# Performance work log

Measured on AMD Instinct MI355X. Metric: run time of the kernel, lower is better.

## Reference

```python
import jax, jax.numpy as jnp
import numpy as np

N_NODES = 50000
N_EDGES = 1_600_000
IN_DIM = 128
HID = 64


def gcn_conv(x, src, dst, w, W, b, n):
    # PyG GCNConv(normalize=True, add_self_loops=True):
    # add self loops with weight 1, sym-normalize, x@W (no bias in lin), scatter-add, +bias
    loop = jnp.arange(n)
    s = jnp.concatenate([src, loop])
    d = jnp.concatenate([dst, loop])
    ww = jnp.concatenate([w, jnp.ones((n,), w.dtype)])
    deg = jax.ops.segment_sum(ww, d, num_segments=n)                 # [n]
    dis = jnp.where(deg > 0, jax.lax.rsqrt(deg), 0.0)                # deg^{-1/2}, inf->0
    norm = dis[s] * ww * dis[d]                                      # [E+n]
    h = x @ W                                                        # [n, out]
    msg = h[s] * norm[:, None]                                       # gather + scale
    out = jax.ops.segment_sum(msg, d, num_segments=n)                # scatter-add at dst
    return out + b


def setup_inputs() -> dict:
    key = jax.random.key(0)
    ks = jax.random.split(key, 9)
    X = jax.random.normal(ks[0], (N_NODES, IN_DIM), dtype=jnp.float32)
    edge_index = jax.random.randint(ks[1], (2, N_EDGES), 0, N_NODES, dtype=jnp.int64)
    edge_weight = jax.random.uniform(ks[2], (N_EDGES,), dtype=jnp.float32)
    s1 = 1.0 / np.sqrt(IN_DIM)
    s2 = 1.0 / np.sqrt(HID)
    W1 = jax.random.uniform(ks[3], (IN_DIM, HID), jnp.float32, -s1, s1)
    b1 = jax.random.uniform(ks[4], (HID,), jnp.float32, -s1, s1)
    W2 = jax.random.uniform(ks[5], (HID, HID), jnp.float32, -s2, s2)
    b2 = jax.random.uniform(ks[6], (HID,), jnp.float32, -s2, s2)
    Wl = jax.random.uniform(ks[7], (HID, 1), jnp.float32, -s2, s2)
    bl = jax.random.uniform(ks[8], (1,), jnp.float32, -s2, s2)
    return {"X": X, "edge_index": edge_index, "edge_weight": edge_weight,
            "W1": W1, "b1": b1, "W2": W2, "b2": b2, "Wl": Wl, "bl": bl}


def reference(X, edge_index, edge_weight, W1, b1, W2, b2, Wl, bl):
    n = X.shape[0]
    src, dst = edge_index[0], edge_index[1]
    h = jax.nn.relu(gcn_conv(X, src, dst, edge_weight, W1, b1, n))
    # F.dropout(p=0.2) is identity in eval mode
    h = jax.nn.relu(gcn_conv(h, src, dst, edge_weight, W2, b2, n))
    return jax.nn.sigmoid(h @ Wl + bl).squeeze(1)   # [n]
```

## Files before the change

kernel.cpp:

```cpp
#include <hip/hip_runtime.h>

typedef float f32x2 __attribute__((ext_vector_type(2)));

#define A2B 1024
#define A2T 512
#define STG 3200

__device__ __forceinline__ long ld_idx(const void* idx, long pos, int is64) {
  return is64 ? (long)((const long long*)idx)[pos]
              : (long)((const int*)idx)[pos];
}

__device__ __forceinline__ int detect_is64(const void* idx) {
  const unsigned long long* p = (const unsigned long long*)idx;
  unsigned long long v = p[threadIdx.x & 63];
  return (__ballot((v >> 32) != 0ull) == 0ull) ? 1 : 0;
}

__device__ __forceinline__ int swz_group(int bid, int GP) {
  int r = bid & 7, q = bid >> 3;
  int j = q / GP;
  int i = q - j * GP;
  return (r + 8 * j) * GP + i;
}

__device__ __forceinline__ void scan256(unsigned* sh, unsigned* wsums, int t) {
  unsigned v = 0;
  if (t < 256) {
    v = sh[t];
#pragma unroll
    for (int off = 1; off < 64; off <<= 1) {
      unsigned u = __shfl_up(v, off, 64);
      if ((t & 63) >= off) v += u;
    }
    if ((t & 63) == 63) wsums[t >> 6] = v;
  }
  __syncthreads();
  if (t < 256) {
    unsigned add = 0;
    int wid = t >> 6;
#pragma unroll
    for (int i = 0; i < 3; ++i) if (i < wid) add += wsums[i];
    sh[t] = v + add;
  }
  __syncthreads();
}

__device__ __forceinline__ uint4 pack16_fp8(const float* acc) {
  uint4 o;
  unsigned v;
  v = 0;
  v = __builtin_amdgcn_cvt_pk_fp8_f32(acc[0],  acc[1],  v, false);
  v = __builtin_amdgcn_cvt_pk_fp8_f32(acc[2],  acc[3],  v, true);
  o.x = v; v = 0;
  v = __builtin_amdgcn_cvt_pk_fp8_f32(acc[4],  acc[5],  v, false);
  v = __builtin_amdgcn_cvt_pk_fp8_f32(acc[6],  acc[7],  v, true);
  o.y = v; v = 0;
  v = __builtin_amdgcn_cvt_pk_fp8_f32(acc[8],  acc[9],  v, false);
  v = __builtin_amdgcn_cvt_pk_fp8_f32(acc[10], acc[11], v, true);
  o.z = v; v = 0;
  v = __builtin_amdgcn_cvt_pk_fp8_f32(acc[12], acc[13], v, false);
  v = __builtin_amdgcn_cvt_pk_fp8_f32(acc[14], acc[15], v, true);
  o.w = v;
  return o;
}

__global__ __launch_bounds__(256) void k_front(const void* __restrict__ idx,
                                               unsigned* __restrict__ histT,
                                               long E, int chunk, unsigned M) {
  __shared__ unsigned cnt[256];
  const int t = threadIdx.x;
  const int b = blockIdx.x;
  const int is64 = detect_is64(idx);
  cnt[t] = 0;
  __syncthreads();
  const long e0 = (long)b * chunk;
  long e1 = e0 + chunk; if (e1 > E) e1 = E;
  for (long e = e0 + t; e < e1; e += 256) {
    unsigned d = (unsigned)ld_idx(idx, E + e, is64);
    atomicAdd(&cnt[__umulhi(d, M)], 1u);
  }
  __syncthreads();
  histT[(size_t)t * A2B + b] = cnt[t];
}

__global__ __launch_bounds__(256) void k_colscan(const unsigned* __restrict__ histT,
                                                 unsigned* __restrict__ baseT,
                                                 unsigned* __restrict__ colsum) {
  __shared__ unsigned sh[256], wsums[4];
  const int k = blockIdx.x, t = threadIdx.x;
  const uint4 v = ((const uint4*)(histT + (size_t)k * A2B))[t];
  unsigned s = v.x + v.y + v.z + v.w;
  sh[t] = s;
  __syncthreads();
  scan256(sh, wsums, t);
  unsigned excl = sh[t] - s;
  uint4 o;
  o.x = excl;
  o.y = excl + v.x;
  o.z = o.y + v.y;
  o.w = o.z + v.z;
  ((uint4*)(baseT + (size_t)k * A2B))[t] = o;
  if (t == 255) colsum[k] = sh[255];
}

__global__ __launch_bounds__(A2T) void k_bucket(const void* __restrict__ idx,
                                                const float* __restrict__ w,
                                                const unsigned* __restrict__ baseT,
                                                const unsigned* __restrict__ colsum,
                                                uint2* __restrict__ recs,
                                                long E, int chunk, unsigned M,
                                                const float* __restrict__ X,
                                                const float* __restrict__ W1,
                                                unsigned char* __restrict__ h, int n) {
  __shared__ uint2 stage[4096];
  __shared__ unsigned cnt[256], lofs[256], lbase[256], bcol[256], scanb[256], wsums[4];
  const int t = threadIdx.x;
  if (blockIdx.x >= A2B) {
    float* Ws = (float*)stage;
    for (int i = t; i < 2048; i += A2T)
      ((float4*)Ws)[i] = ((const float4*)W1)[i];
    __syncthreads();
    int gid = (blockIdx.x - A2B) * A2T + t;
    int node = gid >> 2;
    int fg = (gid & 3) * 16;
    if (node >= n) return;
    const float4* xr4 = (const float4*)(X + (size_t)node * 128);
    float acc[16];
#pragma unroll
    for (int f = 0; f < 16; ++f) acc[f] = 0.0f;
    for (int k4 = 0; k4 < 32; ++k4) {
      float4 x = xr4[k4];
#pragma unroll
      for (int kk = 0; kk < 4; ++kk) {
        float xv = (kk == 0) ? x.x : (kk == 1) ? x.y : (kk == 2) ? x.z : x.w;
        const float4* wrow = (const float4*)(Ws + (k4 * 4 + kk) * 64 + fg);
#pragma unroll
        for (int f4 = 0; f4 < 4; ++f4) {
          float4 wv = wrow[f4];
          acc[f4 * 4 + 0] = fmaf(xv, wv.x, acc[f4 * 4 + 0]);
          acc[f4 * 4 + 1] = fmaf(xv, wv.y, acc[f4 * 4 + 1]);
          acc[f4 * 4 + 2] = fmaf(xv, wv.z, acc[f4 * 4 + 2]);
          acc[f4 * 4 + 3] = fmaf(xv, wv.w, acc[f4 * 4 + 3]);
        }
      }
    }
    *(uint4*)(h + (size_t)node * 64 + fg) = pack16_fp8(acc);
    return;
  }
  const int b = blockIdx.x;
  const long e0 = (long)b * chunk;
  long e1 = e0 + chunk; if (e1 > E) e1 = E;
  const int m = (int)(e1 - e0);
  const int is64 = detect_is64(idx);
  if (t < 256) scanb[t] = colsum[t];
  __syncthreads();
  scan256(scanb, wsums, t);
  if (t < 256) {
    bcol[t] = (scanb[t] - colsum[t]) + baseT[(size_t)t * A2B + b];
    cnt[t] = 0;
  }
  __syncthreads();
  unsigned short dc[4]; unsigned char kc[4];
  int nk = 0;
  for (long e = e0 + t; e < e1; e += A2T, ++nk) {
    unsigned d = (unsigned)ld_idx(idx, E + e, is64);
    unsigned kb = __umulhi(d, M);
    dc[nk] = (unsigned short)d; kc[nk] = (unsigned char)kb;
    atomicAdd(&cnt[kb], 1u);
  }
  __syncthreads();
  if (t < 256) scanb[t] = cnt[t];
  __syncthreads();
  scan256(scanb, wsums, t);
  if (t < 256) { unsigned ex = scanb[t] - cnt[t]; lbase[t] = ex; lofs[t] = ex; }
  __syncthreads();
  nk = 0;
  for (long e = e0 + t; e < e1; e += A2T, ++nk) {
    unsigned s = (unsigned)ld_idx(idx, e, is64);
    float wv = w[e];
    unsigned kb = kc[nk];
    unsigned pos = atomicAdd(&lofs[kb], 1u);
    stage[pos] = make_uint2(s | ((unsigned)dc[nk] << 16), __float_as_uint(wv));
  }
  __syncthreads();
  for (int i = t; i < m; i += A2T) {
    uint2 r = stage[i];
    unsigned kb = __umulhi(r.x >> 16, M);
    recs[bcol[kb] + (unsigned)i - lbase[kb]] = r;
  }
}

__global__ __launch_bounds__(1024) void k_bp(const uint2* __restrict__ recs,
                                             const unsigned* __restrict__ colsum,
                                             int* __restrict__ rowptr,
                                             float* __restrict__ dis,
                                             float2* __restrict__ edges,
                                             int n, int dwidth, long E) {
  __shared__ float wsum[256];
  __shared__ unsigned cnt[256], lofs[256], scanb[256], wsums[4];
  const int k = blockIdx.x, t = threadIdx.x;
  const int d0 = k * dwidth;
  if (t < 256) scanb[t] = colsum[t];
  __syncthreads();
  scan256(scanb, wsums, t);
  const int r1 = (int)scanb[k];
  const int r0 = r1 - (int)colsum[k];
  if (t < 256) { wsum[t] = 0.0f; cnt[t] = 0; }
  __syncthreads();
  const int m = r1 - r0;
  for (int i = t; i < m; i += 1024) {
    uint2 r = recs[r0 + i];
    int dl = (int)(r.x >> 16) - d0;
    atomicAdd(&cnt[dl], 1u);
    atomicAdd(&wsum[dl], __uint_as_float(r.y));
  }
  __syncthreads();
  if (t < 256) scanb[t] = cnt[t];
  __syncthreads();
  scan256(scanb, wsums, t);
  if (t < 256) {
    unsigned ex = scanb[t] - cnt[t];
    lofs[t] = (unsigned)r0 + ex;
    int d = d0 + t;
    if (t < dwidth && d < n) {
      rowptr[d] = r0 + (int)ex;
      dis[d] = rsqrtf(1.0f + wsum[t]);
    }
  }
  if (k == gridDim.x - 1 && t == 0) rowptr[n] = (int)E;
  __syncthreads();
  for (int i = t; i < m; i += 1024) {
    uint2 r = recs[r0 + i];
    unsigned pos = atomicAdd(&lofs[(int)(r.x >> 16) - d0], 1u);
    edges[pos] = make_float2(__uint_as_float(r.x & 0xffffu), __uint_as_float(r.y));
  }
}

__device__ __forceinline__ void gather_acc(const unsigned char* __restrict__ h,
                                           const float* __restrict__ dis,
                                           const float2* __restrict__ edges,
                                           int beg, int end, int eg, int fl,
                                           float* acc) {
  f32x2 a0 = {0.0f, 0.0f}, a1 = {0.0f, 0.0f}, a2 = {0.0f, 0.0f}, a3 = {0.0f, 0.0f};
  const unsigned char* hf = h + fl * 8;
  for (int base = beg; base < end; base += 48) {
    float2 rv[12];
#pragma unroll
    for (int s = 0; s < 12; ++s) {
      int idx = base + s * 4 + eg;
      rv[s] = edges[min(idx, end - 1)];
    }
    int sj[12];
    float nj[12];
#pragma unroll
    for (int s = 0; s < 12; ++s) {
      sj[s] = __float_as_int(rv[s].x);
      nj[s] = rv[s].y * dis[sj[s]];
    }
    uint2 hv[12];
#pragma unroll
    for (int s = 0; s < 12; ++s)
      hv[s] = *(const uint2*)(hf + (size_t)sj[s] * 64);
#pragma unroll
    for (int s = 0; s < 12; ++s) {
      float w = (base + s * 4 + eg < end) ? nj[s] : 0.0f;
      f32x2 nj2 = {w, w};
      a0 += __builtin_amdgcn_cvt_pk_f32_fp8(hv[s].x, false) * nj2;
      a1 += __builtin_amdgcn_cvt_pk_f32_fp8(hv[s].x, true)  * nj2;
      a2 += __builtin_amdgcn_cvt_pk_f32_fp8(hv[s].y, false) * nj2;
      a3 += __builtin_amdgcn_cvt_pk_f32_fp8(hv[s].y, true)  * nj2;
    }
  }
  acc[0] = a0[0]; acc[1] = a0[1]; acc[2] = a1[0]; acc[3] = a1[1];
  acc[4] = a2[0]; acc[5] = a2[1]; acc[6] = a3[0]; acc[7] = a3[1];
#pragma unroll
  for (int off = 8; off < 32; off <<= 1)
#pragma unroll
    for (int i = 0; i < 8; ++i) acc[i] += __shfl_xor(acc[i], off);
}

__device__ __forceinline__ void add_bias_self(const unsigned char* __restrict__ h,
                                              const float* __restrict__ b,
                                              int node, int fl, float s0, float* acc) {
  uint2 hv = *(const uint2*)(h + (size_t)node * 64 + fl * 8);
  f32x2 q0 = __builtin_amdgcn_cvt_pk_f32_fp8(hv.x, false);
  f32x2 q1 = __builtin_amdgcn_cvt_pk_f32_fp8(hv.x, true);
  f32x2 q2 = __builtin_amdgcn_cvt_pk_f32_fp8(hv.y, false);
  f32x2 q3 = __builtin_amdgcn_cvt_pk_f32_fp8(hv.y, true);
  float hs[8] = {q0[0], q0[1], q1[0], q1[1], q2[0], q2[1], q3[0], q3[1]};
  float4 bv0 = *(const float4*)(b + fl * 8);
  float4 bv1 = *(const float4*)(b + fl * 8 + 4);
  float bb[8] = {bv0.x, bv0.y, bv0.z, bv0.w, bv1.x, bv1.y, bv1.z, bv1.w};
  float s2 = s0 * s0;
#pragma unroll
  for (int i = 0; i < 8; ++i) acc[i] += bb[i] + hs[i] * s2;
}

__global__ __launch_bounds__(256) void k_gather_mid(const unsigned char* __restrict__ h,
                                                    const float* __restrict__ dis,
                                                    const float2* __restrict__ edges,
                                                    const int* __restrict__ rowptr,
                                                    const float* __restrict__ b1,
                                                    const float* __restrict__ W2,
                                                    unsigned char* __restrict__ h2,
                                                    int n, int GP) {
  __shared__ float W2s[64 * 64];
  __shared__ float xs[8 * 64];
  const int t = threadIdx.x;
  for (int i = t; i < 1024; i += 256)
    ((float4*)W2s)[i] = ((const float4*)W2)[i];
  int lane = t & 63;
  int l32 = lane & 31;
  int fl = lane & 7;
  int eg = (lane >> 3) & 3;
  int nl = t >> 5;
  const int g = swz_group(blockIdx.x, GP);
  int node = g * 8 + nl;
  int beg = 0, end = 0; float s0 = 0.0f;
  if (node < n) { beg = rowptr[node]; end = rowptr[node + 1]; s0 = dis[node]; }
  float acc[8];
  gather_acc(h, dis, edges, beg, end, eg, fl, acc);
  if (node < n) {
#pragma unroll
    for (int i = 0; i < 8; ++i) acc[i] *= s0;
    add_bias_self(h, b1, node, fl, s0, acc);
    if (eg == 0) {
#pragma unroll
      for (int i = 0; i < 8; ++i) xs[nl * 64 + fl * 8 + i] = fmaxf(acc[i], 0.0f);
    }
  }
  __syncthreads();
  int tl = l32;
  int node2 = g * 8 + (t >> 5);
  if (node2 >= n) return;
  const float* xrow = xs + (t >> 5) * 64;
  int f = tl * 2;
  float a0 = 0.0f, a1 = 0.0f;
#pragma unroll 8
  for (int k = 0; k < 64; ++k) {
    float xk = xrow[k];
    f32x2 wv = *(const f32x2*)(W2s + k * 64 + f);
    a0 = fmaf(xk, wv[0], a0);
    a1 = fmaf(xk, wv[1], a1);
  }
  unsigned v = __builtin_amdgcn_cvt_pk_fp8_f32(a0, a1, 0u, false);
  *(unsigned short*)(h2 + (size_t)node2 * 64 + f) = (unsigned short)v;
}

__global__ __launch_bounds__(256) void k_gather_fin(const unsigned char* __restrict__ h,
                                                    const float* __restrict__ dis,
                                                    const float2* __restrict__ edges,
                                                    const int* __restrict__ rowptr,
                                                    const float* __restrict__ b2,
                                                    const float* __restrict__ Wl,
                                                    const float* __restrict__ bl,
                                                    float* __restrict__ out,
                                                    int n, int GP) {
  int lane = threadIdx.x & 63;
  int l32 = lane & 31;
  int fl = lane & 7;
  int eg = (lane >> 3) & 3;
  const int g = swz_group(blockIdx.x, GP);
  int node = g * 8 + (int)(threadIdx.x >> 5);
  if (node >= n) return;
  int beg = rowptr[node], end = rowptr[node + 1];
  float s0 = dis[node];
  float acc[8];
  gather_acc(h, dis, edges, beg, end, eg, fl, acc);
#pragma unroll
  for (int i = 0; i < 8; ++i) acc[i] *= s0;
  add_bias_self(h, b2, node, fl, s0, acc);
  float4 wl0 = *(const float4*)(Wl + fl * 8);
  float4 wl1 = *(const float4*)(Wl + fl * 8 + 4);
  float wl[8] = {wl0.x, wl0.y, wl0.z, wl0.w, wl1.x, wl1.y, wl1.z, wl1.w};
  float v = 0.0f;
#pragma unroll
  for (int i = 0; i < 8; ++i) v += fmaxf(acc[i], 0.0f) * wl[i];
#pragma unroll
  for (int off = 1; off < 8; off <<= 1) v += __shfl_xor(v, off);
  if (l32 == 0) out[node] = 1.0f / (1.0f + expf(-(v + bl[0])));
}

extern "C" void kernel_launch(void* const* d_in, const int* in_sizes, int n_in,
                              void* d_out, int out_size, void* d_ws, size_t ws_size,
                              hipStream_t stream) {
  const float* X  = (const float*)d_in[0];
  const void*  EI = d_in[1];
  const float* EW = (const float*)d_in[2];
  const float* W1 = (const float*)d_in[3];
  const float* b1 = (const float*)d_in[4];
  const float* W2 = (const float*)d_in[5];
  const float* b2 = (const float*)d_in[6];
  const float* Wl = (const float*)d_in[7];
  const float* bl = (const float*)d_in[8];
  float* out = (float*)d_out;

  const int  n = in_sizes[0] / 128;
  const long E = (long)in_sizes[1] / 2;

  const int chunk  = (int)((E + A2B - 1) / A2B);
  const int dwidth = (((n + 255) / 256) + 7) & ~7;
  const int GP     = dwidth >> 3;
  const unsigned M = (unsigned)((0x100000000ULL + (unsigned)dwidth - 1) / (unsigned)dwidth);

  auto align = [](size_t x) { return (x + 255) & ~(size_t)255; };
  char* ws = (char*)d_ws;
  size_t off = 0;
  float*         dis    = (float*)(ws + off);         off += align((size_t)n * 4);
  int*           rowptr = (int*)(ws + off);           off += align((size_t)(n + 1) * 4);
  unsigned*      colsum = (unsigned*)(ws + off);      off += align(256 * 4);
  unsigned*      histT  = (unsigned*)(ws + off);      off += align((size_t)A2B * 256 * 4);
  unsigned*      baseT  = (unsigned*)(ws + off);      off += align((size_t)A2B * 256 * 4);
  uint2*         recs   = (uint2*)(ws + off);         off += align((size_t)E * 8);
  float2*        edges  = (float2*)(ws + off);        off += align((size_t)E * 8);
  unsigned char* A      = (unsigned char*)(ws + off); off += align((size_t)n * 64);
  unsigned char* A2     = (unsigned char*)(ws + off); off += align((size_t)n * 64);

  const int nbW  = 32 * dwidth;
  const int nbG  = (n * 4 + A2T - 1) / A2T;

  k_front<<<A2B, dim3(256), 0, stream>>>(EI, histT, E, chunk, M);
  k_colscan<<<256, 256, 0, stream>>>(histT, baseT, colsum);
  k_bucket<<<A2B + nbG, dim3(A2T), 0, stream>>>(EI, EW, baseT, colsum, recs, E, chunk, M,
                                                X, W1, A, n);
  k_bp<<<256, dim3(1024), 0, stream>>>(recs, colsum, rowptr, dis, edges, n, dwidth, E);

  k_gather_mid<<<nbW, dim3(256), 0, stream>>>(A, dis, edges, rowptr, b1, W2, A2, n, GP);
  k_gather_fin<<<nbW, dim3(256), 0, stream>>>(A2, dis, edges, rowptr, b2, Wl, bl, out, n, GP);
}
```

Baseline: 214.8 us.

## Fuse graph preprocessing kernels into one cooperative kernel with grid syncs

Merges the histogram, column scan, bucket scatter and per-bucket CSR build kernels into a single cooperative launch, separated by grid.sync() barriers. The X@W1 projection is folded into the first phase of the first blocks. The edge chunking drops from 1024 to 512 blocks of 512 threads, so each block handles about twice as many edges. The aim is to remove kernel launch gaps and inter-kernel drain, at the cost of grid-wide barrier overhead, lower block-level parallelism, and the matmul now sitting in front of the first barrier.

```diff
diff --git a/kernel.cpp b/kernel.cpp
--- a/kernel.cpp
+++ b/kernel.cpp
@@ -1,9 +1,12 @@
 #include <hip/hip_runtime.h>
+#include <hip/hip_cooperative_groups.h>
+
+namespace cg = cooperative_groups;
 
 typedef float f32x2 __attribute__((ext_vector_type(2)));
 
-#define A2B 1024
-#define A2T 512
+#define A2B 512
+#define CPT 512
 #define STG 3200
 
 __device__ __forceinline__ long ld_idx(const void* idx, long pos, int is64) {
@@ -65,94 +68,93 @@
   return o;
 }
 
-__global__ __launch_bounds__(256) void k_front(const void* __restrict__ idx,
-                                               unsigned* __restrict__ histT,
-                                               long E, int chunk, unsigned M) {
-  __shared__ unsigned cnt[256];
+__global__ __launch_bounds__(CPT, 4) void k_prep(const void* __restrict__ idx,
+                                                 const float* __restrict__ w,
+                                                 unsigned* __restrict__ histT,
+                                                 unsigned* __restrict__ baseT,
+                                                 unsigned* __restrict__ colsum,
+                                                 uint2* __restrict__ recs,
+                                                 int* __restrict__ rowptr,
+                                                 float* __restrict__ dis,
+                                                 float2* __restrict__ edges,
+                                                 const float* __restrict__ X,
+                                                 const float* __restrict__ W1,
+                                                 unsigned char* __restrict__ h,
+                                                 long E, int chunk, unsigned M,
+                                                 int n, int dwidth, int nbG1) {
+  __shared__ uint2 stage[4096];
+  __shared__ unsigned cnt[256], lofs[256], lbase[256], bcol[256], scanb[256], wsums[8];
+  __shared__ float wsum[256];
+  cg::grid_group grid = cg::this_grid();
   const int t = threadIdx.x;
   const int b = blockIdx.x;
   const int is64 = detect_is64(idx);
-  cnt[t] = 0;
-  __syncthreads();
-  const long e0 = (long)b * chunk;
-  long e1 = e0 + chunk; if (e1 > E) e1 = E;
-  for (long e = e0 + t; e < e1; e += 256) {
-    unsigned d = (unsigned)ld_idx(idx, E + e, is64);
-    atomicAdd(&cnt[__umulhi(d, M)], 1u);
-  }
-  __syncthreads();
-  histT[(size_t)t * A2B + b] = cnt[t];
-}
-
-__global__ __launch_bounds__(256) void k_colscan(const unsigned* __restrict__ histT,
-                                                 unsigned* __restrict__ baseT,
-                                                 unsigned* __restrict__ colsum) {
-  __shared__ unsigned sh[256], wsums[4];
-  const int k = blockIdx.x, t = threadIdx.x;
-  const uint4 v = ((const uint4*)(histT + (size_t)k * A2B))[t];
-  unsigned s = v.x + v.y + v.z + v.w;
-  sh[t] = s;
-  __syncthreads();
-  scan256(sh, wsums, t);
-  unsigned excl = sh[t] - s;
-  uint4 o;
-  o.x = excl;
-  o.y = excl + v.x;
-  o.z = o.y + v.y;
-  o.w = o.z + v.z;
-  ((uint4*)(baseT + (size_t)k * A2B))[t] = o;
-  if (t == 255) colsum[k] = sh[255];
-}
-
-__global__ __launch_bounds__(A2T) void k_bucket(const void* __restrict__ idx,
-                                                const float* __restrict__ w,
-                                                const unsigned* __restrict__ baseT,
-                                                const unsigned* __restrict__ colsum,
-                                                uint2* __restrict__ recs,
-                                                long E, int chunk, unsigned M,
-                                                const float* __restrict__ X,
-                                                const float* __restrict__ W1,
-                                                unsigned char* __restrict__ h, int n) {
-  __shared__ uint2 stage[4096];
-  __shared__ unsigned cnt[256], lofs[256], lbase[256], bcol[256], scanb[256], wsums[4];
-  const int t = threadIdx.x;
-  if (blockIdx.x >= A2B) {
-    float* Ws = (float*)stage;
-    for (int i = t; i < 2048; i += A2T)
-      ((float4*)Ws)[i] = ((const float4*)W1)[i];
-    __syncthreads();
-    int gid = (blockIdx.x - A2B) * A2T + t;
-    int node = gid >> 2;
-    int fg = (gid & 3) * 16;
-    if (node >= n) return;
-    const float4* xr4 = (const float4*)(X + (size_t)node * 128);
-    float acc[16];
-#pragma unroll
-    for (int f = 0; f < 16; ++f) acc[f] = 0.0f;
-    for (int k4 = 0; k4 < 32; ++k4) {
-      float4 x = xr4[k4];
-#pragma unroll
-      for (int kk = 0; kk < 4; ++kk) {
-        float xv = (kk == 0) ? x.x : (kk == 1) ? x.y : (kk == 2) ? x.z : x.w;
-        const float4* wrow = (const float4*)(Ws + (k4 * 4 + kk) * 64 + fg);
-#pragma unroll
-        for (int f4 = 0; f4 < 4; ++f4) {
-          float4 wv = wrow[f4];
-          acc[f4 * 4 + 0] = fmaf(xv, wv.x, acc[f4 * 4 + 0]);
-          acc[f4 * 4 + 1] = fmaf(xv, wv.y, acc[f4 * 4 + 1]);
-          acc[f4 * 4 + 2] = fmaf(xv, wv.z, acc[f4 * 4 + 2]);
-          acc[f4 * 4 + 3] = fmaf(xv, wv.w, acc[f4 * 4 + 3]);
-        }
-      }
-    }
-    *(uint4*)(h + (size_t)node * 64 + fg) = pack16_fp8(acc);
-    return;
-  }
-  const int b = blockIdx.x;
   const long e0 = (long)b * chunk;
   long e1 = e0 + chunk; if (e1 > E) e1 = E;
   const int m = (int)(e1 - e0);
-  const int is64 = detect_is64(idx);
+
+  if (t < 256) cnt[t] = 0;
+  __syncthreads();
+  for (long e = e0 + t; e < e1; e += CPT) {
+    unsigned d = (unsigned)ld_idx(idx, E + e, is64);
+    atomicAdd(&cnt[__umulhi(d, M)], 1u);
+  }
+  __syncthreads();
+  if (t < 256) histT[(size_t)t * A2B + b] = cnt[t];
+  if (b < nbG1) {
+    float* Ws = (float*)stage;
+    for (int i = t; i < 2048; i += CPT)
+      ((float4*)Ws)[i] = ((const float4*)W1)[i];
+    __syncthreads();
+    int gid = b * CPT + t;
+    int node = gid >> 2;
+    int fg = (gid & 3) * 16;
+    if (node < n) {
+      const float4* xr4 = (const float4*)(X + (size_t)node * 128);
+      float acc[16];
+#pragma unroll
+      for (int f = 0; f < 16; ++f) acc[f] = 0.0f;
+      for (int k4 = 0; k4 < 32; ++k4) {
+        float4 x = xr4[k4];
+#pragma unroll
+        for (int kk = 0; kk < 4; ++kk) {
+          float xv = (kk == 0) ? x.x : (kk == 1) ? x.y : (kk == 2) ? x.z : x.w;
+          const float4* wrow = (const float4*)(Ws + (k4 * 4 + kk) * 64 + fg);
+#pragma unroll
+          for (int f4 = 0; f4 < 4; ++f4) {
+            float4 wv = wrow[f4];
+            acc[f4 * 4 + 0] = fmaf(xv, wv.x, acc[f4 * 4 + 0]);
+            acc[f4 * 4 + 1] = fmaf(xv, wv.y, acc[f4 * 4 + 1]);
+            acc[f4 * 4 + 2] = fmaf(xv, wv.z, acc[f4 * 4 + 2]);
+            acc[f4 * 4 + 3] = fmaf(xv, wv.w, acc[f4 * 4 + 3]);
+          }
+        }
+      }
+      *(uint4*)(h + (size_t)node * 64 + fg) = pack16_fp8(acc);
+    }
+  }
+  grid.sync();
+
+  if (b < 256) {
+    unsigned hv = histT[(size_t)b * A2B + t];
+    unsigned v = hv;
+#pragma unroll
+    for (int off = 1; off < 64; off <<= 1) {
+      unsigned u = __shfl_up(v, off, 64);
+      if ((t & 63) >= off) v += u;
+    }
+    if ((t & 63) == 63) wsums[t >> 6] = v;
+    __syncthreads();
+    unsigned add = 0;
+    int wid = t >> 6;
+#pragma unroll
+    for (int i = 0; i < 7; ++i) if (i < wid) add += wsums[i];
+    v += add;
+    baseT[(size_t)b * A2B + t] = v - hv;
+    if (t == CPT - 1) colsum[b] = v;
+  }
+  grid.sync();
+
   if (t < 256) scanb[t] = colsum[t];
   __syncthreads();
   scan256(scanb, wsums, t);
@@ -161,9 +163,9 @@
     cnt[t] = 0;
   }
   __syncthreads();
-  unsigned short dc[4]; unsigned char kc[4];
+  unsigned short dc[8]; unsigned char kc[8];
   int nk = 0;
-  for (long e = e0 + t; e < e1; e += A2T, ++nk) {
+  for (long e = e0 + t; e < e1; e += CPT, ++nk) {
     unsigned d = (unsigned)ld_idx(idx, E + e, is64);
     unsigned kb = __umulhi(d, M);
     dc[nk] = (unsigned short)d; kc[nk] = (unsigned char)kb;
@@ -176,7 +178,7 @@
   if (t < 256) { unsigned ex = scanb[t] - cnt[t]; lbase[t] = ex; lofs[t] = ex; }
   __syncthreads();
   nk = 0;
-  for (long e = e0 + t; e < e1; e += A2T, ++nk) {
+  for (long e = e0 + t; e < e1; e += CPT, ++nk) {
     unsigned s = (unsigned)ld_idx(idx, e, is64);
     float wv = w[e];
     unsigned kb = kc[nk];
@@ -184,56 +186,49 @@
     stage[pos] = make_uint2(s | ((unsigned)dc[nk] << 16), __float_as_uint(wv));
   }
   __syncthreads();
-  for (int i = t; i < m; i += A2T) {
+  for (int i = t; i < m; i += CPT) {
     uint2 r = stage[i];
     unsigned kb = __umulhi(r.x >> 16, M);
     recs[bcol[kb] + (unsigned)i - lbase[kb]] = r;
   }
-}
-
-__global__ __launch_bounds__(1024) void k_bp(const uint2* __restrict__ recs,
-                                             const unsigned* __restrict__ colsum,
-                                             int* __restrict__ rowptr,
-                                             float* __restrict__ dis,
-                                             float2* __restrict__ edges,
-                                             int n, int dwidth, long E) {
-  __shared__ float wsum[256];
-  __shared__ unsigned cnt[256], lofs[256], scanb[256], wsums[4];
-  const int k = blockIdx.x, t = threadIdx.x;
-  const int d0 = k * dwidth;
-  if (t < 256) scanb[t] = colsum[t];
-  __syncthreads();
-  scan256(scanb, wsums, t);
-  const int r1 = (int)scanb[k];
-  const int r0 = r1 - (int)colsum[k];
-  if (t < 256) { wsum[t] = 0.0f; cnt[t] = 0; }
-  __syncthreads();
-  const int m = r1 - r0;
-  for (int i = t; i < m; i += 1024) {
-    uint2 r = recs[r0 + i];
-    int dl = (int)(r.x >> 16) - d0;
-    atomicAdd(&cnt[dl], 1u);
-    atomicAdd(&wsum[dl], __uint_as_float(r.y));
-  }
-  __syncthreads();
-  if (t < 256) scanb[t] = cnt[t];
-  __syncthreads();
-  scan256(scanb, wsums, t);
-  if (t < 256) {
-    unsigned ex = scanb[t] - cnt[t];
-    lofs[t] = (unsigned)r0 + ex;
-    int d = d0 + t;
-    if (t < dwidth && d < n) {
-      rowptr[d] = r0 + (int)ex;
-      dis[d] = rsqrtf(1.0f + wsum[t]);
-    }
-  }
-  if (k == gridDim.x - 1 && t == 0) rowptr[n] = (int)E;
-  __syncthreads();
-  for (int i = t; i < m; i += 1024) {
-    uint2 r = recs[r0 + i];
-    unsigned pos = atomicAdd(&lofs[(int)(r.x >> 16) - d0], 1u);
-    edges[pos] = make_float2(__uint_as_float(r.x & 0xffffu), __uint_as_float(r.y));
+  grid.sync();
+
+  if (b < 256) {
+    const int d0 = b * dwidth;
+    if (t < 256) scanb[t] = colsum[t];
+    __syncthreads();
+    scan256(scanb, wsums, t);
+    const int r1 = (int)scanb[b];
+    const int r0 = r1 - (int)colsum[b];
+    if (t < 256) { wsum[t] = 0.0f; cnt[t] = 0; }
+    __syncthreads();
+    const int mm = r1 - r0;
+    for (int i = t; i < mm; i += CPT) {
+      uint2 r = recs[r0 + i];
+      int dl = (int)(r.x >> 16) - d0;
+      atomicAdd(&cnt[dl], 1u);
+      atomicAdd(&wsum[dl], __uint_as_float(r.y));
+    }
+    __syncthreads();
+    if (t < 256) scanb[t] = cnt[t];
+    __syncthreads();
+    scan256(scanb, wsums, t);
+    if (t < 256) {
+      unsigned ex = scanb[t] - cnt[t];
+      lofs[t] = (unsigned)r0 + ex;
+      int d = d0 + t;
+      if (t < dwidth && d < n) {
+        rowptr[d] = r0 + (int)ex;
+        dis[d] = rsqrtf(1.0f + wsum[t]);
+      }
+    }
+    if (b == 255 && t == 0) rowptr[n] = (int)E;
+    __syncthreads();
+    for (int i = t; i < mm; i += CPT) {
+      uint2 r = recs[r0 + i];
+      unsigned pos = atomicAdd(&lofs[(int)(r.x >> 16) - d0], 1u);
+      edges[pos] = make_float2(__uint_as_float(r.x & 0xffffu), __uint_as_float(r.y));
+    }
   }
 }
 
@@ -418,13 +413,17 @@
   unsigned char* A2     = (unsigned char*)(ws + off); off += align((size_t)n * 64);
 
   const int nbW  = 32 * dwidth;
-  const int nbG  = (n * 4 + A2T - 1) / A2T;
-
-  k_front<<<A2B, dim3(256), 0, stream>>>(EI, histT, E, chunk, M);
-  k_colscan<<<256, 256, 0, stream>>>(histT, baseT, colsum);
-  k_bucket<<<A2B + nbG, dim3(A2T), 0, stream>>>(EI, EW, baseT, colsum, recs, E, chunk, M,
-                                                X, W1, A, n);
-  k_bp<<<256, dim3(1024), 0, stream>>>(recs, colsum, rowptr, dis, edges, n, dwidth, E);
+  int nbG1 = (n * 4 + CPT - 1) / CPT;
+
+  long  E_ = E;
+  int   chunk_ = chunk, n_ = n, dwidth_ = dwidth;
+  unsigned M_ = M;
+  void* args[] = {(void*)&EI, (void*)&EW, (void*)&histT, (void*)&baseT, (void*)&colsum,
+                  (void*)&recs, (void*)&rowptr, (void*)&dis, (void*)&edges,
+                  (void*)&X, (void*)&W1, (void*)&A,
+                  (void*)&E_, (void*)&chunk_, (void*)&M_,
+                  (void*)&n_, (void*)&dwidth_, (void*)&nbG1};
+  hipLaunchCooperativeKernel((const void*)k_prep, dim3(A2B), dim3(CPT), args, 0, stream);
 
   k_gather_mid<<<nbW, dim3(256), 0, stream>>>(A, dis, edges, rowptr, b1, W2, A2, n, GP);
   k_gather_fin<<<nbW, dim3(256), 0, stream>>>(A2, dis, edges, rowptr, b2, Wl, bl, out, n, GP);
```

After: 404.2 us. +88.1%, slower.

## Fuse column scan into histogram via last-block ticket, halve bucket blocks, move degree sum

Applied to the files above, without the earlier changes.

Removes the separate k_colscan launch: the last k_front block, picked with an atomic ticket, does a serial per-row scan of the histogram to produce baseT and colsum. The bucket block count drops from 1024 to 512, which doubles the edges per block and the per-thread register arrays. In k_bp the float shared-memory atomic for weighted degree is replaced by a 4-lane segmented reduction over the already sorted edges. Costs added are a memset launch, a serial 512-length scan done by one block, and a second read of the edges array.

```diff
diff --git a/kernel.cpp b/kernel.cpp
--- a/kernel.cpp
+++ b/kernel.cpp
@@ -2,7 +2,7 @@
 
 typedef float f32x2 __attribute__((ext_vector_type(2)));
 
-#define A2B 1024
+#define A2B 512
 #define A2T 512
 #define STG 3200
 
@@ -67,8 +67,12 @@
 
 __global__ __launch_bounds__(256) void k_front(const void* __restrict__ idx,
                                                unsigned* __restrict__ histT,
+                                               unsigned* __restrict__ baseT,
+                                               unsigned* __restrict__ colsum,
+                                               unsigned* __restrict__ ticket,
                                                long E, int chunk, unsigned M) {
   __shared__ unsigned cnt[256];
+  __shared__ unsigned rank_s;
   const int t = threadIdx.x;
   const int b = blockIdx.x;
   const int is64 = detect_is64(idx);
@@ -82,26 +86,21 @@
   }
   __syncthreads();
   histT[(size_t)t * A2B + b] = cnt[t];
-}
-
-__global__ __launch_bounds__(256) void k_colscan(const unsigned* __restrict__ histT,
-                                                 unsigned* __restrict__ baseT,
-                                                 unsigned* __restrict__ colsum) {
-  __shared__ unsigned sh[256], wsums[4];
-  const int k = blockIdx.x, t = threadIdx.x;
-  const uint4 v = ((const uint4*)(histT + (size_t)k * A2B))[t];
-  unsigned s = v.x + v.y + v.z + v.w;
-  sh[t] = s;
-  __syncthreads();
-  scan256(sh, wsums, t);
-  unsigned excl = sh[t] - s;
-  uint4 o;
-  o.x = excl;
-  o.y = excl + v.x;
-  o.z = o.y + v.y;
-  o.w = o.z + v.z;
-  ((uint4*)(baseT + (size_t)k * A2B))[t] = o;
-  if (t == 255) colsum[k] = sh[255];
+  __threadfence();
+  if (t == 0) rank_s = atomicAdd(ticket, 1u);
+  __syncthreads();
+  if (rank_s != A2B - 1) return;
+  __threadfence();
+  const unsigned* row = histT + (size_t)t * A2B;
+  unsigned* brow = baseT + (size_t)t * A2B;
+  unsigned run = 0;
+#pragma unroll 8
+  for (int j = 0; j < A2B; ++j) {
+    unsigned hv = row[j];
+    brow[j] = run;
+    run += hv;
+  }
+  colsum[t] = run;
 }
 
 __global__ __launch_bounds__(A2T) void k_bucket(const void* __restrict__ idx,
@@ -161,7 +160,7 @@
     cnt[t] = 0;
   }
   __syncthreads();
-  unsigned short dc[4]; unsigned char kc[4];
+  unsigned short dc[8]; unsigned char kc[8];
   int nk = 0;
   for (long e = e0 + t; e < e1; e += A2T, ++nk) {
     unsigned d = (unsigned)ld_idx(idx, E + e, is64);
@@ -197,7 +196,6 @@
                                              float* __restrict__ dis,
                                              float2* __restrict__ edges,
                                              int n, int dwidth, long E) {
-  __shared__ float wsum[256];
   __shared__ unsigned cnt[256], lofs[256], scanb[256], wsums[4];
   const int k = blockIdx.x, t = threadIdx.x;
   const int d0 = k * dwidth;
@@ -206,14 +204,12 @@
   scan256(scanb, wsums, t);
   const int r1 = (int)scanb[k];
   const int r0 = r1 - (int)colsum[k];
-  if (t < 256) { wsum[t] = 0.0f; cnt[t] = 0; }
+  if (t < 256) cnt[t] = 0;
   __syncthreads();
   const int m = r1 - r0;
   for (int i = t; i < m; i += 1024) {
     uint2 r = recs[r0 + i];
-    int dl = (int)(r.x >> 16) - d0;
-    atomicAdd(&cnt[dl], 1u);
-    atomicAdd(&wsum[dl], __uint_as_float(r.y));
+    atomicAdd(&cnt[(int)(r.x >> 16) - d0], 1u);
   }
   __syncthreads();
   if (t < 256) scanb[t] = cnt[t];
@@ -223,10 +219,7 @@
     unsigned ex = scanb[t] - cnt[t];
     lofs[t] = (unsigned)r0 + ex;
     int d = d0 + t;
-    if (t < dwidth && d < n) {
-      rowptr[d] = r0 + (int)ex;
-      dis[d] = rsqrtf(1.0f + wsum[t]);
-    }
+    if (t < dwidth && d < n) rowptr[d] = r0 + (int)ex;
   }
   if (k == gridDim.x - 1 && t == 0) rowptr[n] = (int)E;
   __syncthreads();
@@ -234,6 +227,20 @@
     uint2 r = recs[r0 + i];
     unsigned pos = atomicAdd(&lofs[(int)(r.x >> 16) - d0], 1u);
     edges[pos] = make_float2(__uint_as_float(r.x & 0xffffu), __uint_as_float(r.y));
+  }
+  __syncthreads();
+  int nid = t >> 2, ln = t & 3;
+  if (nid < dwidth) {
+    int d = d0 + nid;
+    if (d < n) {
+      int a  = r0 + (int)(scanb[nid] - cnt[nid]);
+      int bn = r0 + (int)scanb[nid];
+      float s = 0.0f;
+      for (int i = a + ln; i < bn; i += 4) s += edges[i].y;
+      s += __shfl_xor(s, 1);
+      s += __shfl_xor(s, 2);
+      if (ln == 0) dis[d] = rsqrtf(1.0f + s);
+    }
   }
 }
 
@@ -410,6 +417,7 @@
   float*         dis    = (float*)(ws + off);         off += align((size_t)n * 4);
   int*           rowptr = (int*)(ws + off);           off += align((size_t)(n + 1) * 4);
   unsigned*      colsum = (unsigned*)(ws + off);      off += align(256 * 4);
+  unsigned*      ticket = (unsigned*)(ws + off);      off += align(4);
   unsigned*      histT  = (unsigned*)(ws + off);      off += align((size_t)A2B * 256 * 4);
   unsigned*      baseT  = (unsigned*)(ws + off);      off += align((size_t)A2B * 256 * 4);
   uint2*         recs   = (uint2*)(ws + off);         off += align((size_t)E * 8);
@@ -420,8 +428,9 @@
   const int nbW  = 32 * dwidth;
   const int nbG  = (n * 4 + A2T - 1) / A2T;
 
-  k_front<<<A2B, dim3(256), 0, stream>>>(EI, histT, E, chunk, M);
-  k_colscan<<<256, 256, 0, stream>>>(histT, baseT, colsum);
+  hipMemsetAsync(ticket, 0, 4, stream);
+
+  k_front<<<A2B, dim3(256), 0, stream>>>(EI, histT, baseT, colsum, ticket, E, chunk, M);
   k_bucket<<<A2B + nbG, dim3(A2T), 0, stream>>>(EI, EW, baseT, colsum, recs, E, chunk, M,
                                                 X, W1, A, n);
   k_bp<<<256, dim3(1024), 0, stream>>>(recs, colsum, rowptr, dis, edges, n, dwidth, E);
```

New measurement: 316.2 us. 1.47x slower.
